# Optimization experiments

Hardware: AMD Instinct MI355X
Metric: run time of the kernel (lower is better)

Reference implementation:

```python
import jax, jax.numpy as jnp
import numpy as np

NO_FEATURES = 512
NO_HEADS = 8
HEAD_DIM = NO_FEATURES // NO_HEADS


def setup_inputs() -> dict:
    key = jax.random.key(0)
    ks = jax.random.split(key, 10)
    B, S, D = 4, 2048, NO_FEATURES
    s = 1.0 / np.sqrt(D)
    return {
        "x": jax.random.normal(ks[0], (B, S, D), dtype=jnp.float32),
        "ln_gamma": jnp.ones((D,), jnp.float32),
        "ln_beta": jnp.zeros((D,), jnp.float32),
        "Wq": jax.random.uniform(ks[1], (D, D), jnp.float32, -s, s),
        "bq": jax.random.uniform(ks[2], (D,), jnp.float32, -s, s),
        "Wk": jax.random.uniform(ks[3], (D, D), jnp.float32, -s, s),
        "bk": jax.random.uniform(ks[4], (D,), jnp.float32, -s, s),
        "Wv": jax.random.uniform(ks[5], (D, D), jnp.float32, -s, s),
        "bv": jax.random.uniform(ks[6], (D,), jnp.float32, -s, s),
        "Wo": jax.random.uniform(ks[7], (D, D), jnp.float32, -s, s),
        "bo": jax.random.uniform(ks[8], (D,), jnp.float32, -s, s),
    }


def reference(x, ln_gamma, ln_beta, Wq, bq, Wk, bk, Wv, bv, Wo, bo):
    B, S, D = x.shape
    H, Dh = NO_HEADS, D // NO_HEADS
    # Pre-LayerNorm (eps = 1e-5, torch default)
    mu = jnp.mean(x, axis=-1, keepdims=True)
    var = jnp.mean(jnp.square(x - mu), axis=-1, keepdims=True)
    xn = (x - mu) * jax.lax.rsqrt(var + 1e-5) * ln_gamma + ln_beta
    # QKV projections (torch Linear: x @ W.T + b)
    q = (xn @ Wq.T + bq).reshape(B, S, H, Dh).transpose(0, 2, 1, 3)
    k = (xn @ Wk.T + bk).reshape(B, S, H, Dh).transpose(0, 2, 1, 3)
    v = (xn @ Wv.T + bv).reshape(B, S, H, Dh).transpose(0, 2, 1, 3)
    scale = Dh ** -0.5
    scores = jnp.einsum("bhqd,bhkd->bhqk", q, k) * scale  # [B,H,S,S]
    attn = jax.nn.softmax(scores, axis=-1)
    # dropout is identity in eval mode
    out = jnp.einsum("bhqk,bhkd->bhqd", attn, v)
    out = out.transpose(0, 2, 1, 3).reshape(B, S, D)
    return out @ Wo.T + bo
```

## Files before the change

### kernel.cpp

```cpp
#include <hip/hip_runtime.h>
#include <cstdint>
#include <cstddef>

#define NB 4
#define NS 2048
#define ND 512
#define NH 8
#define DH 64
#define MTOK (NB*NS)

typedef __bf16 bf16x8 __attribute__((ext_vector_type(8)));
typedef float f32x4 __attribute__((ext_vector_type(4)));
typedef float f32x16 __attribute__((ext_vector_type(16)));
typedef unsigned int u32x4 __attribute__((ext_vector_type(4)));
typedef unsigned short ushort_t;
typedef unsigned int uint_t;

__device__ __forceinline__ unsigned short f2bf(float f) {
  unsigned int u = __builtin_bit_cast(unsigned int, f);
  return (unsigned short)((u + 0x7fffu + ((u >> 16) & 1u)) >> 16);
}

__device__ __forceinline__ uint_t cvtpk(float lo, float hi) {
  uint_t r;
  asm("v_cvt_pk_bf16_f32 %0, %1, %2" : "=v"(r) : "v"(lo), "v"(hi));
  return r;
}

__device__ __forceinline__ void pswap(uint_t &a, uint_t &b) {
  asm("v_permlane32_swap_b32 %0, %1" : "+v"(a), "+v"(b));
}

__device__ __forceinline__ void gload_lds16(const void* g, void* l) {
  __builtin_amdgcn_global_load_lds(
      (const __attribute__((address_space(1))) unsigned int*)g,
      (__attribute__((address_space(3))) unsigned int*)l,
      16, 0, 0);
}

__device__ __forceinline__ bf16x8 ld8(const ushort_t* p) { return *(const bf16x8*)p; }

__global__ __launch_bounds__(256) void ln_kernel(
    const float* __restrict__ x, const float* __restrict__ gamma,
    const float* __restrict__ beta, ushort_t* __restrict__ xn)
{
  const int row  = blockIdx.x * 4 + (threadIdx.x >> 6);
  const int lane = threadIdx.x & 63;
  const float4* xr = (const float4*)(x + (size_t)row * ND);
  float4 a = xr[lane*2], b = xr[lane*2+1];
  float v[8] = {a.x,a.y,a.z,a.w,b.x,b.y,b.z,b.w};
  float s = 0.f, s2 = 0.f;
#pragma unroll
  for (int j = 0; j < 8; ++j) { s += v[j]; s2 += v[j]*v[j]; }
#pragma unroll
  for (int mk = 1; mk < 64; mk <<= 1) { s += __shfl_xor(s, mk); s2 += __shfl_xor(s2, mk); }
  const float mu = s * (1.0f/ND);
  const float rs = rsqrtf(s2*(1.0f/ND) - mu*mu + 1e-5f);
  const float4* g4 = (const float4*)gamma;
  const float4* b4 = (const float4*)beta;
  float4 g0 = g4[lane*2], g1 = g4[lane*2+1];
  float4 e0 = b4[lane*2], e1 = b4[lane*2+1];
  float gv[8] = {g0.x,g0.y,g0.z,g0.w,g1.x,g1.y,g1.z,g1.w};
  float ev[8] = {e0.x,e0.y,e0.z,e0.w,e1.x,e1.y,e1.z,e1.w};
  unsigned short o[8];
#pragma unroll
  for (int j = 0; j < 8; ++j) o[j] = f2bf((v[j]-mu)*rs*gv[j] + ev[j]);
  uint4 ov;
  ov.x = (uint_t)o[0] | ((uint_t)o[1]<<16);
  ov.y = (uint_t)o[2] | ((uint_t)o[3]<<16);
  ov.z = (uint_t)o[4] | ((uint_t)o[5]<<16);
  ov.w = (uint_t)o[6] | ((uint_t)o[7]<<16);
  ((uint4*)(xn + (size_t)row*ND))[lane] = ov;
}

__global__ __launch_bounds__(256) void convert_w(
    const float* __restrict__ Wq, const float* __restrict__ Wk,
    const float* __restrict__ Wv, const float* __restrict__ Wo,
    ushort_t* __restrict__ wqkv, ushort_t* __restrict__ wob)
{
  const int t = blockIdx.x*256 + threadIdx.x;
  const int i = t*8;
  const float* src; ushort_t* dst;
  if (i < 1536*512) {
    const int n = i >> 9, c = i & 511;
    const float* W = (n < 512) ? Wq : (n < 1024) ? Wk : Wv;
    src = W + ((size_t)(n & 511) << 9) + c;
    dst = wqkv + i;
  } else {
    const int jj = i - 1536*512;
    src = Wo + jj; dst = wob + jj;
  }
  float4 a = ((const float4*)src)[0], b = ((const float4*)src)[1];
  uint4 o;
  o.x = (uint_t)f2bf(a.x) | ((uint_t)f2bf(a.y)<<16);
  o.y = (uint_t)f2bf(a.z) | ((uint_t)f2bf(a.w)<<16);
  o.z = (uint_t)f2bf(b.x) | ((uint_t)f2bf(b.y)<<16);
  o.w = (uint_t)f2bf(b.z) | ((uint_t)f2bf(b.w)<<16);
  *(uint4*)dst = o;
}

template<int EPI>
__global__ __launch_bounds__(256, 2) void gemm_bt(
    const ushort_t* __restrict__ A, const ushort_t* __restrict__ Bw, int Kd,
    const float* __restrict__ bq, const float* __restrict__ bk, const float* __restrict__ bv,
    ushort_t* __restrict__ qa, ushort_t* __restrict__ ka, ushort_t* __restrict__ vta,
    const float* __restrict__ bo, float* __restrict__ outp)
{
  __shared__ ushort_t lA[128*32];
  __shared__ ushort_t lB[128*32];
  const int tid = threadIdx.x;
  const int wave = tid >> 6, lane = tid & 63;
  const int m0 = blockIdx.y * 128, n0 = blockIdx.x * 128;
  const int wr = (wave >> 1) * 64, wc = (wave & 1) * 64;

  f32x4 acc[4][4] = {};

  const ushort_t* aS = A  + (size_t)(m0 + tid/4) * Kd + (tid & 3) * 8;
  const ushort_t* bS = Bw + (size_t)(n0 + tid/4) * Kd + (tid & 3) * 8;
  const size_t half = (size_t)64 * Kd;

  for (int k0 = 0; k0 < Kd; k0 += 32) {
    __syncthreads();
    gload_lds16(aS + k0,        lA + wave*512);
    gload_lds16(aS + half + k0, lA + 2048 + wave*512);
    gload_lds16(bS + k0,        lB + wave*512);
    gload_lds16(bS + half + k0, lB + 2048 + wave*512);
    __syncthreads();
    bf16x8 af[4], bfr[4];
#pragma unroll
    for (int i = 0; i < 4; ++i)
      af[i] = *(const bf16x8*)(lA + (wr + i*16 + (lane&15))*32 + (lane>>4)*8);
#pragma unroll
    for (int j = 0; j < 4; ++j)
      bfr[j] = *(const bf16x8*)(lB + (wc + j*16 + (lane&15))*32 + (lane>>4)*8);
#pragma unroll
    for (int i = 0; i < 4; ++i)
#pragma unroll
      for (int j = 0; j < 4; ++j)
        acc[i][j] = __builtin_amdgcn_mfma_f32_16x16x32_bf16(af[i], bfr[j], acc[i][j], 0, 0, 0);
  }

  if (EPI == 0) {
    const float QSCALE = 0.18033688011112042f;
#pragma unroll
    for (int j = 0; j < 4; ++j) {
      const int n = n0 + wc + j*16 + (lane & 15);
      const int which = n >> 9;
      const int nn = n & 511;
      const int h = nn >> 6, d = nn & 63;
      const float bb = (which == 0) ? bq[nn] : (which == 1) ? bk[nn] : bv[nn];
#pragma unroll
      for (int i = 0; i < 4; ++i)
#pragma unroll
        for (int r = 0; r < 4; ++r) {
          const int mm = m0 + wr + i*16 + 4*(lane>>4) + r;
          const int b = mm >> 11, s = mm & 2047;
          const int bh = b*NH + h;
          const float av = acc[i][j][r] + bb;
          if (which == 0) {
            qa[(((size_t)bh*64 + (s>>5))*4 + (d>>4))*512
               + (((d>>3)&1)*32 + (s&31))*8 + (d&7)] = f2bf(av * QSCALE);
          } else if (which == 1) {
            ka[(((size_t)bh*64 + (s>>5))*4 + (d>>4))*512
               + (((d>>3)&1)*32 + (s&31))*8 + (d&7)] = f2bf(av);
          } else {
            vta[(((size_t)bh*128 + (s>>4))*2 + (d>>5))*512
               + (((s>>3)&1)*32 + (d&31))*8 + (s&7)] = f2bf(av);
          }
        }
    }
  } else {
#pragma unroll
    for (int j = 0; j < 4; ++j) {
      const int n = n0 + wc + j*16 + (lane & 15);
      const float bb = bo[n];
#pragma unroll
      for (int i = 0; i < 4; ++i)
#pragma unroll
        for (int r = 0; r < 4; ++r) {
          const int m = m0 + wr + i*16 + 4*(lane>>4) + r;
          outp[(size_t)m*ND + n] = acc[i][j][r] + bb;
        }
    }
  }
}

__global__ __launch_bounds__(256) void attn_kernel(
    const ushort_t* __restrict__ qfv, const ushort_t* __restrict__ kfv,
    const ushort_t* __restrict__ vfv, ushort_t* __restrict__ ao)
{
  const int blk  = blockIdx.x;
  const int bh   = (blk & 7) | ((blk >> 7) << 3);
  const int qblk = (blk >> 3) & 15;
  const int w    = threadIdx.x >> 6;
  const int lane = threadIdx.x & 63;
  const int lo5 = lane & 31, hi = lane >> 5;
  const int qt = qblk*4 + w;

  const ushort_t* qb = qfv + (((size_t)bh*64 + qt)*4)*512 + lane*8;
  bf16x8 qf[4];
#pragma unroll
  for (int s = 0; s < 4; ++s) qf[s] = ld8(qb + s*512);

  const ushort_t* kb = kfv + ((size_t)bh*64*4)*512 + lane*8;
  const ushort_t* vb = vfv + ((size_t)bh*128*2)*512 + lane*8;

  f32x16 o0 = {}, o1 = {};
  float l0 = 0.f, l1 = 0.f, l2 = 0.f, l3 = 0.f;

  bf16x8 kf0[4], kf1[4];
#pragma unroll
  for (int s = 0; s < 4; ++s) {
    kf0[s] = ld8(kb + (size_t)s*512);
    kf1[s] = ld8(kb + (size_t)(4+s)*512);
  }

  for (int j0 = 0; j0 < NS; j0 += 64) {
    bf16x8 vf0[4], vf1[4];
    const int kv16 = j0 >> 4;
#pragma unroll
    for (int ks = 0; ks < 4; ++ks) {
      vf0[ks] = ld8(vb + ((size_t)(kv16+ks)*2    )*512);
      vf1[ks] = ld8(vb + ((size_t)(kv16+ks)*2 + 1)*512);
    }
    f32x16 s0 = {}, s1 = {};
#pragma unroll
    for (int s = 0; s < 4; ++s) {
      s0 = __builtin_amdgcn_mfma_f32_32x32x16_bf16(kf0[s], qf[s], s0, 0, 0, 0);
      s1 = __builtin_amdgcn_mfma_f32_32x32x16_bf16(kf1[s], qf[s], s1, 0, 0, 0);
    }
    if (j0 + 64 < NS) {
      const int kt = (j0 >> 5) + 2;
#pragma unroll
      for (int s = 0; s < 4; ++s) {
        kf0[s] = ld8(kb + ((size_t)(kt  )*4 + s)*512);
        kf1[s] = ld8(kb + ((size_t)(kt+1)*4 + s)*512);
      }
    }
#pragma unroll
    for (int r = 0; r < 16; r += 4) {
      s0[r]   = __builtin_amdgcn_exp2f(s0[r]);   l0 += s0[r];
      s0[r+1] = __builtin_amdgcn_exp2f(s0[r+1]); l1 += s0[r+1];
      s0[r+2] = __builtin_amdgcn_exp2f(s0[r+2]); l2 += s0[r+2];
      s0[r+3] = __builtin_amdgcn_exp2f(s0[r+3]); l3 += s0[r+3];
    }
#pragma unroll
    for (int r = 0; r < 16; r += 4) {
      s1[r]   = __builtin_amdgcn_exp2f(s1[r]);   l0 += s1[r];
      s1[r+1] = __builtin_amdgcn_exp2f(s1[r+1]); l1 += s1[r+1];
      s1[r+2] = __builtin_amdgcn_exp2f(s1[r+2]); l2 += s1[r+2];
      s1[r+3] = __builtin_amdgcn_exp2f(s1[r+3]); l3 += s1[r+3];
    }
    bf16x8 pf[4];
    {
      uint_t a, b, c, d;
      a = cvtpk(s0[0],  s0[1]);  b = cvtpk(s0[4],  s0[5]);  pswap(a, b);
      c = cvtpk(s0[2],  s0[3]);  d = cvtpk(s0[6],  s0[7]);  pswap(c, d);
      pf[0] = __builtin_bit_cast(bf16x8, (u32x4){a, c, b, d});
      a = cvtpk(s0[8],  s0[9]);  b = cvtpk(s0[12], s0[13]); pswap(a, b);
      c = cvtpk(s0[10], s0[11]); d = cvtpk(s0[14], s0[15]); pswap(c, d);
      pf[1] = __builtin_bit_cast(bf16x8, (u32x4){a, c, b, d});
      a = cvtpk(s1[0],  s1[1]);  b = cvtpk(s1[4],  s1[5]);  pswap(a, b);
      c = cvtpk(s1[2],  s1[3]);  d = cvtpk(s1[6],  s1[7]);  pswap(c, d);
      pf[2] = __builtin_bit_cast(bf16x8, (u32x4){a, c, b, d});
      a = cvtpk(s1[8],  s1[9]);  b = cvtpk(s1[12], s1[13]); pswap(a, b);
      c = cvtpk(s1[10], s1[11]); d = cvtpk(s1[14], s1[15]); pswap(c, d);
      pf[3] = __builtin_bit_cast(bf16x8, (u32x4){a, c, b, d});
    }
#pragma unroll
    for (int ks = 0; ks < 4; ++ks) {
      o0 = __builtin_amdgcn_mfma_f32_32x32x16_bf16(vf0[ks], pf[ks], o0, 0, 0, 0);
      o1 = __builtin_amdgcn_mfma_f32_32x32x16_bf16(vf1[ks], pf[ks], o1, 0, 0, 0);
    }
  }

  float l = (l0 + l1) + (l2 + l3);
  l += __shfl_xor(l, 32);
  const float rl = __builtin_amdgcn_rcpf(l);
  const int b = bh >> 3, h = bh & 7;
  const int srow = qt*32 + lo5;
  ushort_t* ob = ao + ((size_t)(b*NS + srow))*ND + h*DH;
#pragma unroll
  for (int dt = 0; dt < 2; ++dt) {
    f32x16& oo = dt ? o1 : o0;
#pragma unroll
    for (int r = 0; r < 16; r += 2) {
      const int d = (r & 3) + 8*(r >> 2) + 4*hi + dt*32;
      *(uint_t*)(ob + d) = cvtpk(oo[r]*rl, oo[r+1]*rl);
    }
  }
}

extern "C" void kernel_launch(void* const* d_in, const int* in_sizes, int n_in,
                              void* d_out, int out_size, void* d_ws, size_t ws_size,
                              hipStream_t stream)
{
  const float* x  = (const float*)d_in[0];
  const float* g  = (const float*)d_in[1];
  const float* be = (const float*)d_in[2];
  const float* Wq = (const float*)d_in[3];
  const float* bq = (const float*)d_in[4];
  const float* Wk = (const float*)d_in[5];
  const float* bk = (const float*)d_in[6];
  const float* Wv = (const float*)d_in[7];
  const float* bv = (const float*)d_in[8];
  const float* Wo = (const float*)d_in[9];
  const float* bo = (const float*)d_in[10];
  float* out = (float*)d_out;

  char* w = (char*)d_ws;
  ushort_t* xn   = (ushort_t*)w; w += (size_t)MTOK*ND*2;
  ushort_t* wqkv = (ushort_t*)w; w += (size_t)1536*512*2;
  ushort_t* wob  = (ushort_t*)w; w += (size_t)512*512*2;
  ushort_t* qa   = (ushort_t*)w; w += (size_t)MTOK*ND*2;
  ushort_t* ka   = (ushort_t*)w; w += (size_t)MTOK*ND*2;
  ushort_t* vta  = (ushort_t*)w; w += (size_t)MTOK*ND*2;
  ushort_t* ao   = (ushort_t*)w; w += (size_t)MTOK*ND*2;

  ln_kernel<<<MTOK/4, 256, 0, stream>>>(x, g, be, xn);
  convert_w<<<512, 256, 0, stream>>>(Wq, Wk, Wv, Wo, wqkv, wob);
  gemm_bt<0><<<dim3(12, 64), 256, 0, stream>>>(xn, wqkv, ND,
      bq, bk, bv, qa, ka, vta, nullptr, nullptr);
  attn_kernel<<<512, 256, 0, stream>>>(qa, ka, vta, ao);
  gemm_bt<1><<<dim3(4, 64), 256, 0, stream>>>(ao, wob, ND,
      nullptr, nullptr, nullptr, nullptr, nullptr, nullptr, bo, out);
}
```

Measured before the change: 100.9 us.

## Split attention over the key dimension into two halves with a combine pass

The attention kernel now splits each head's key range in two, launching twice as many blocks. Each block writes unnormalised fp32 partial outputs and row sums. A new combine kernel adds the partials, normalises them and writes bf16 output into the reused Q buffer; the final output buffer serves as scratch for one partial. This raises block count to fill more compute units, at the cost of extra fp32 traffic and one more launch. No running max is kept, which is fine because the pre-split code also skipped max subtraction.

```diff
diff --git a/kernel.cpp b/kernel.cpp
--- a/kernel.cpp
+++ b/kernel.cpp
@@ -8,6 +8,7 @@
 #define NH 8
 #define DH 64
 #define MTOK (NB*NS)
+#define NROW (NB*NH*NS)
 
 typedef __bf16 bf16x8 __attribute__((ext_vector_type(8)));
 typedef float f32x4 __attribute__((ext_vector_type(4)));
@@ -187,13 +188,15 @@
 
 __global__ __launch_bounds__(256) void attn_kernel(
     const ushort_t* __restrict__ qfv, const ushort_t* __restrict__ kfv,
-    const ushort_t* __restrict__ vfv, ushort_t* __restrict__ ao)
-{
-  const int blk  = blockIdx.x;
-  const int bh   = (blk & 7) | ((blk >> 7) << 3);
-  const int qblk = (blk >> 3) & 15;
-  const int w    = threadIdx.x >> 6;
-  const int lane = threadIdx.x & 63;
+    const ushort_t* __restrict__ vfv, float* __restrict__ op0,
+    float* __restrict__ op1, float* __restrict__ lsum)
+{
+  const int blk   = blockIdx.x;
+  const int bh    = (blk & 7) | ((blk >> 8) << 3);
+  const int qblk  = (blk >> 3) & 15;
+  const int split = (blk >> 7) & 1;
+  const int w     = threadIdx.x >> 6;
+  const int lane  = threadIdx.x & 63;
   const int lo5 = lane & 31, hi = lane >> 5;
   const int qt = qblk*4 + w;
 
@@ -202,8 +205,8 @@
 #pragma unroll
   for (int s = 0; s < 4; ++s) qf[s] = ld8(qb + s*512);
 
-  const ushort_t* kb = kfv + ((size_t)bh*64*4)*512 + lane*8;
-  const ushort_t* vb = vfv + ((size_t)bh*128*2)*512 + lane*8;
+  const ushort_t* kb = kfv + ((size_t)bh*256 + split*128)*512 + lane*8;
+  const ushort_t* vb = vfv + ((size_t)bh*256 + split*128)*512 + lane*8;
 
   f32x16 o0 = {}, o1 = {};
   float l0 = 0.f, l1 = 0.f, l2 = 0.f, l3 = 0.f;
@@ -215,7 +218,7 @@
     kf1[s] = ld8(kb + (size_t)(4+s)*512);
   }
 
-  for (int j0 = 0; j0 < NS; j0 += 64) {
+  for (int j0 = 0; j0 < NS/2; j0 += 64) {
     bf16x8 vf0[4], vf1[4];
     const int kv16 = j0 >> 4;
 #pragma unroll
@@ -229,7 +232,7 @@
       s0 = __builtin_amdgcn_mfma_f32_32x32x16_bf16(kf0[s], qf[s], s0, 0, 0, 0);
       s1 = __builtin_amdgcn_mfma_f32_32x32x16_bf16(kf1[s], qf[s], s1, 0, 0, 0);
     }
-    if (j0 + 64 < NS) {
+    if (j0 + 64 < NS/2) {
       const int kt = (j0 >> 5) + 2;
 #pragma unroll
       for (int s = 0; s < 4; ++s) {
@@ -276,19 +279,39 @@
 
   float l = (l0 + l1) + (l2 + l3);
   l += __shfl_xor(l, 32);
-  const float rl = __builtin_amdgcn_rcpf(l);
-  const int b = bh >> 3, h = bh & 7;
-  const int srow = qt*32 + lo5;
-  ushort_t* ob = ao + ((size_t)(b*NS + srow))*ND + h*DH;
+  const int row = bh*NS + qt*32 + lo5;
+  float* ob = (split ? op1 : op0) + (size_t)row * DH;
 #pragma unroll
   for (int dt = 0; dt < 2; ++dt) {
     f32x16& oo = dt ? o1 : o0;
 #pragma unroll
     for (int r = 0; r < 16; r += 2) {
       const int d = (r & 3) + 8*(r >> 2) + 4*hi + dt*32;
-      *(uint_t*)(ob + d) = cvtpk(oo[r]*rl, oo[r+1]*rl);
-    }
-  }
+      float2 v2; v2.x = oo[r]; v2.y = oo[r+1];
+      *(float2*)(ob + d) = v2;
+    }
+  }
+  if (hi == 0) lsum[(size_t)split*NROW + row] = l;
+}
+
+__global__ __launch_bounds__(256) void combine_kernel(
+    const float* __restrict__ op0, const float* __restrict__ op1,
+    const float* __restrict__ lsum, ushort_t* __restrict__ ao)
+{
+  const int t = blockIdx.x*256 + threadIdx.x;
+  const int row = t >> 3, d8 = (t & 7) * 8;
+  const float rl = 1.0f / (lsum[row] + lsum[NROW + row]);
+  const float4 a0 = *(const float4*)(op0 + (size_t)row*DH + d8);
+  const float4 a1 = *(const float4*)(op0 + (size_t)row*DH + d8 + 4);
+  const float4 b0 = *(const float4*)(op1 + (size_t)row*DH + d8);
+  const float4 b1 = *(const float4*)(op1 + (size_t)row*DH + d8 + 4);
+  u32x4 o;
+  o[0] = cvtpk((a0.x+b0.x)*rl, (a0.y+b0.y)*rl);
+  o[1] = cvtpk((a0.z+b0.z)*rl, (a0.w+b0.w)*rl);
+  o[2] = cvtpk((a1.x+b1.x)*rl, (a1.y+b1.y)*rl);
+  o[3] = cvtpk((a1.z+b1.z)*rl, (a1.w+b1.w)*rl);
+  const int bh = row >> 11, s = row & 2047, bb = bh >> 3, h = bh & 7;
+  *(u32x4*)(ao + ((size_t)(bb*NS + s))*ND + h*DH + d8) = o;
 }
 
 extern "C" void kernel_launch(void* const* d_in, const int* in_sizes, int n_in,
@@ -315,13 +338,17 @@
   ushort_t* qa   = (ushort_t*)w; w += (size_t)MTOK*ND*2;
   ushort_t* ka   = (ushort_t*)w; w += (size_t)MTOK*ND*2;
   ushort_t* vta  = (ushort_t*)w; w += (size_t)MTOK*ND*2;
-  ushort_t* ao   = (ushort_t*)w; w += (size_t)MTOK*ND*2;
+  float*    lsum = (float*)w;    w += (size_t)2*NROW*4;
+  float*    op1  = (float*)w;    w += (size_t)NROW*DH*4;
+  float* op0 = (float*)d_out;
+  ushort_t* ao = qa;
 
   ln_kernel<<<MTOK/4, 256, 0, stream>>>(x, g, be, xn);
   convert_w<<<512, 256, 0, stream>>>(Wq, Wk, Wv, Wo, wqkv, wob);
   gemm_bt<0><<<dim3(12, 64), 256, 0, stream>>>(xn, wqkv, ND,
       bq, bk, bv, qa, ka, vta, nullptr, nullptr);
-  attn_kernel<<<512, 256, 0, stream>>>(qa, ka, vta, ao);
+  attn_kernel<<<1024, 256, 0, stream>>>(qa, ka, vta, op0, op1, lsum);
+  combine_kernel<<<NROW*8/256, 256, 0, stream>>>(op0, op1, lsum, ao);
   gemm_bt<1><<<dim3(4, 64), 256, 0, stream>>>(ao, wob, ND,
       nullptr, nullptr, nullptr, nullptr, nullptr, nullptr, bo, out);
 }
```

Measured after the change: 109.5 us. 1.08x slower.

## Software-pipeline attention loop: overlap next QK MFMA with current softmax and PV

Applied to the files above, without the earlier changes.

Restructures the attention inner loop into a two-stage software pipeline with double-buffered score accumulators, so the QK^T MFMA for the next KV tile is issued before the exp/pack and PV MFMA of the current tile. K and V fragment loads are also moved to sit between pipeline stages. The aim is to hide MFMA latency behind the VALU softmax work and to keep loads in flight for longer. In exchange, register pressure rises from the extra score accumulators, which could cut occupancy or cause spills.

```diff
diff --git a/kernel.cpp b/kernel.cpp
--- a/kernel.cpp
+++ b/kernel.cpp
@@ -185,6 +185,70 @@
   }
 }
 
+__device__ __forceinline__ void load_k(bf16x8* kf0, bf16x8* kf1,
+                                       const ushort_t* kb, int t) {
+#pragma unroll
+  for (int s = 0; s < 4; ++s) {
+    kf0[s] = ld8(kb + ((size_t)(8*t + s))*512);
+    kf1[s] = ld8(kb + ((size_t)(8*t + 4 + s))*512);
+  }
+}
+__device__ __forceinline__ void load_v(bf16x8* vf0, bf16x8* vf1,
+                                       const ushort_t* vb, int t) {
+#pragma unroll
+  for (int ks = 0; ks < 4; ++ks) {
+    vf0[ks] = ld8(vb + ((size_t)(4*t + ks)*2    )*512);
+    vf1[ks] = ld8(vb + ((size_t)(4*t + ks)*2 + 1)*512);
+  }
+}
+__device__ __forceinline__ void qk_step(f32x16& s0, f32x16& s1,
+    const bf16x8* kf0, const bf16x8* kf1, const bf16x8* qf) {
+  s0 = {}; s1 = {};
+#pragma unroll
+  for (int s = 0; s < 4; ++s) {
+    s0 = __builtin_amdgcn_mfma_f32_32x32x16_bf16(kf0[s], qf[s], s0, 0, 0, 0);
+    s1 = __builtin_amdgcn_mfma_f32_32x32x16_bf16(kf1[s], qf[s], s1, 0, 0, 0);
+  }
+}
+__device__ __forceinline__ void softmax_pack(f32x16& s0, f32x16& s1, bf16x8* pf,
+    float& l0, float& l1, float& l2, float& l3) {
+#pragma unroll
+  for (int r = 0; r < 16; r += 4) {
+    s0[r]   = __builtin_amdgcn_exp2f(s0[r]);   l0 += s0[r];
+    s0[r+1] = __builtin_amdgcn_exp2f(s0[r+1]); l1 += s0[r+1];
+    s0[r+2] = __builtin_amdgcn_exp2f(s0[r+2]); l2 += s0[r+2];
+    s0[r+3] = __builtin_amdgcn_exp2f(s0[r+3]); l3 += s0[r+3];
+  }
+#pragma unroll
+  for (int r = 0; r < 16; r += 4) {
+    s1[r]   = __builtin_amdgcn_exp2f(s1[r]);   l0 += s1[r];
+    s1[r+1] = __builtin_amdgcn_exp2f(s1[r+1]); l1 += s1[r+1];
+    s1[r+2] = __builtin_amdgcn_exp2f(s1[r+2]); l2 += s1[r+2];
+    s1[r+3] = __builtin_amdgcn_exp2f(s1[r+3]); l3 += s1[r+3];
+  }
+  uint_t a, b, c, d;
+  a = cvtpk(s0[0],  s0[1]);  b = cvtpk(s0[4],  s0[5]);  pswap(a, b);
+  c = cvtpk(s0[2],  s0[3]);  d = cvtpk(s0[6],  s0[7]);  pswap(c, d);
+  pf[0] = __builtin_bit_cast(bf16x8, (u32x4){a, c, b, d});
+  a = cvtpk(s0[8],  s0[9]);  b = cvtpk(s0[12], s0[13]); pswap(a, b);
+  c = cvtpk(s0[10], s0[11]); d = cvtpk(s0[14], s0[15]); pswap(c, d);
+  pf[1] = __builtin_bit_cast(bf16x8, (u32x4){a, c, b, d});
+  a = cvtpk(s1[0],  s1[1]);  b = cvtpk(s1[4],  s1[5]);  pswap(a, b);
+  c = cvtpk(s1[2],  s1[3]);  d = cvtpk(s1[6],  s1[7]);  pswap(c, d);
+  pf[2] = __builtin_bit_cast(bf16x8, (u32x4){a, c, b, d});
+  a = cvtpk(s1[8],  s1[9]);  b = cvtpk(s1[12], s1[13]); pswap(a, b);
+  c = cvtpk(s1[10], s1[11]); d = cvtpk(s1[14], s1[15]); pswap(c, d);
+  pf[3] = __builtin_bit_cast(bf16x8, (u32x4){a, c, b, d});
+}
+__device__ __forceinline__ void pv_step(f32x16& o0, f32x16& o1,
+    const bf16x8* vf0, const bf16x8* vf1, const bf16x8* pf) {
+#pragma unroll
+  for (int ks = 0; ks < 4; ++ks) {
+    o0 = __builtin_amdgcn_mfma_f32_32x32x16_bf16(vf0[ks], pf[ks], o0, 0, 0, 0);
+    o1 = __builtin_amdgcn_mfma_f32_32x32x16_bf16(vf1[ks], pf[ks], o1, 0, 0, 0);
+  }
+}
+
 __global__ __launch_bounds__(256) void attn_kernel(
     const ushort_t* __restrict__ qfv, const ushort_t* __restrict__ kfv,
     const ushort_t* __restrict__ vfv, ushort_t* __restrict__ ao)
@@ -202,76 +266,49 @@
 #pragma unroll
   for (int s = 0; s < 4; ++s) qf[s] = ld8(qb + s*512);
 
-  const ushort_t* kb = kfv + ((size_t)bh*64*4)*512 + lane*8;
-  const ushort_t* vb = vfv + ((size_t)bh*128*2)*512 + lane*8;
+  const ushort_t* kb = kfv + ((size_t)bh*256)*512 + lane*8;
+  const ushort_t* vb = vfv + ((size_t)bh*256)*512 + lane*8;
 
   f32x16 o0 = {}, o1 = {};
+  f32x16 sA0 = {}, sA1 = {}, sB0 = {}, sB1 = {};
   float l0 = 0.f, l1 = 0.f, l2 = 0.f, l3 = 0.f;
-
-  bf16x8 kf0[4], kf1[4];
-#pragma unroll
-  for (int s = 0; s < 4; ++s) {
-    kf0[s] = ld8(kb + (size_t)s*512);
-    kf1[s] = ld8(kb + (size_t)(4+s)*512);
-  }
-
-  for (int j0 = 0; j0 < NS; j0 += 64) {
-    bf16x8 vf0[4], vf1[4];
-    const int kv16 = j0 >> 4;
-#pragma unroll
-    for (int ks = 0; ks < 4; ++ks) {
-      vf0[ks] = ld8(vb + ((size_t)(kv16+ks)*2    )*512);
-      vf1[ks] = ld8(vb + ((size_t)(kv16+ks)*2 + 1)*512);
-    }
-    f32x16 s0 = {}, s1 = {};
-#pragma unroll
-    for (int s = 0; s < 4; ++s) {
-      s0 = __builtin_amdgcn_mfma_f32_32x32x16_bf16(kf0[s], qf[s], s0, 0, 0, 0);
-      s1 = __builtin_amdgcn_mfma_f32_32x32x16_bf16(kf1[s], qf[s], s1, 0, 0, 0);
-    }
-    if (j0 + 64 < NS) {
-      const int kt = (j0 >> 5) + 2;
-#pragma unroll
-      for (int s = 0; s < 4; ++s) {
-        kf0[s] = ld8(kb + ((size_t)(kt  )*4 + s)*512);
-        kf1[s] = ld8(kb + ((size_t)(kt+1)*4 + s)*512);
-      }
-    }
-#pragma unroll
-    for (int r = 0; r < 16; r += 4) {
-      s0[r]   = __builtin_amdgcn_exp2f(s0[r]);   l0 += s0[r];
-      s0[r+1] = __builtin_amdgcn_exp2f(s0[r+1]); l1 += s0[r+1];
-      s0[r+2] = __builtin_amdgcn_exp2f(s0[r+2]); l2 += s0[r+2];
-      s0[r+3] = __builtin_amdgcn_exp2f(s0[r+3]); l3 += s0[r+3];
-    }
-#pragma unroll
-    for (int r = 0; r < 16; r += 4) {
-      s1[r]   = __builtin_amdgcn_exp2f(s1[r]);   l0 += s1[r];
-      s1[r+1] = __builtin_amdgcn_exp2f(s1[r+1]); l1 += s1[r+1];
-      s1[r+2] = __builtin_amdgcn_exp2f(s1[r+2]); l2 += s1[r+2];
-      s1[r+3] = __builtin_amdgcn_exp2f(s1[r+3]); l3 += s1[r+3];
-    }
+  bf16x8 kf0[4], kf1[4], vf0[4], vf1[4];
+
+  load_k(kf0, kf1, kb, 0);
+  load_v(vf0, vf1, vb, 0);
+  qk_step(sA0, sA1, kf0, kf1, qf);
+  load_k(kf0, kf1, kb, 1);
+
+  for (int i = 0; i < 15; ++i) {
+    const int t = 2*i;
+    qk_step(sB0, sB1, kf0, kf1, qf);
+    load_k(kf0, kf1, kb, t+2);
+    {
+      bf16x8 pf[4];
+      softmax_pack(sA0, sA1, pf, l0, l1, l2, l3);
+      pv_step(o0, o1, vf0, vf1, pf);
+    }
+    load_v(vf0, vf1, vb, t+1);
+    qk_step(sA0, sA1, kf0, kf1, qf);
+    load_k(kf0, kf1, kb, t+3);
+    {
+      bf16x8 pf[4];
+      softmax_pack(sB0, sB1, pf, l0, l1, l2, l3);
+      pv_step(o0, o1, vf0, vf1, pf);
+    }
+    load_v(vf0, vf1, vb, t+2);
+  }
+  qk_step(sB0, sB1, kf0, kf1, qf);
+  {
     bf16x8 pf[4];
-    {
-      uint_t a, b, c, d;
-      a = cvtpk(s0[0],  s0[1]);  b = cvtpk(s0[4],  s0[5]);  pswap(a, b);
-      c = cvtpk(s0[2],  s0[3]);  d = cvtpk(s0[6],  s0[7]);  pswap(c, d);
-      pf[0] = __builtin_bit_cast(bf16x8, (u32x4){a, c, b, d});
-      a = cvtpk(s0[8],  s0[9]);  b = cvtpk(s0[12], s0[13]); pswap(a, b);
-      c = cvtpk(s0[10], s0[11]); d = cvtpk(s0[14], s0[15]); pswap(c, d);
-      pf[1] = __builtin_bit_cast(bf16x8, (u32x4){a, c, b, d});
-      a = cvtpk(s1[0],  s1[1]);  b = cvtpk(s1[4],  s1[5]);  pswap(a, b);
-      c = cvtpk(s1[2],  s1[3]);  d = cvtpk(s1[6],  s1[7]);  pswap(c, d);
-      pf[2] = __builtin_bit_cast(bf16x8, (u32x4){a, c, b, d});
-      a = cvtpk(s1[8],  s1[9]);  b = cvtpk(s1[12], s1[13]); pswap(a, b);
-      c = cvtpk(s1[10], s1[11]); d = cvtpk(s1[14], s1[15]); pswap(c, d);
-      pf[3] = __builtin_bit_cast(bf16x8, (u32x4){a, c, b, d});
-    }
-#pragma unroll
-    for (int ks = 0; ks < 4; ++ks) {
-      o0 = __builtin_amdgcn_mfma_f32_32x32x16_bf16(vf0[ks], pf[ks], o0, 0, 0, 0);
-      o1 = __builtin_amdgcn_mfma_f32_32x32x16_bf16(vf1[ks], pf[ks], o1, 0, 0, 0);
-    }
+    softmax_pack(sA0, sA1, pf, l0, l1, l2, l3);
+    pv_step(o0, o1, vf0, vf1, pf);
+  }
+  load_v(vf0, vf1, vb, 31);
+  {
+    bf16x8 pf[4];
+    softmax_pack(sB0, sB1, pf, l0, l1, l2, l3);
+    pv_step(o0, o1, vf0, vf1, pf);
   }
 
   float l = (l0 + l1) + (l2 + l3);
```

Result: no change. 101.4 us (+0.5%).

## Double-buffer GEMM LDS tiles and add MFMA priority hints in attention

Applied to the files above, without the earlier changes.

The projection GEMM now keeps two LDS buffers and issues the next K-tile's global-to-LDS loads before computing on the current one. It waits with explicit vmcnt/lgkmcnt counts and raw barriers instead of two __syncthreads per iteration, so load latency can overlap the MFMA work. The attention kernel wraps its MFMA groups in s_setprio, seeds the first score MFMA from a zero constant, and accumulates the row sums as a vector add. The costs are double the GEMM LDS use, which may affect occupancy at 2 blocks per CU, and correctness that depends on hand-written waitcnt values.

```diff
diff --git a/kernel.cpp b/kernel.cpp
--- a/kernel.cpp
+++ b/kernel.cpp
@@ -106,8 +106,8 @@
     ushort_t* __restrict__ qa, ushort_t* __restrict__ ka, ushort_t* __restrict__ vta,
     const float* __restrict__ bo, float* __restrict__ outp)
 {
-  __shared__ ushort_t lA[128*32];
-  __shared__ ushort_t lB[128*32];
+  __shared__ ushort_t lA[2][128*32];
+  __shared__ ushort_t lB[2][128*32];
   const int tid = threadIdx.x;
   const int wave = tid >> 6, lane = tid & 63;
   const int m0 = blockIdx.y * 128, n0 = blockIdx.x * 128;
@@ -118,27 +118,43 @@
   const ushort_t* aS = A  + (size_t)(m0 + tid/4) * Kd + (tid & 3) * 8;
   const ushort_t* bS = Bw + (size_t)(n0 + tid/4) * Kd + (tid & 3) * 8;
   const size_t half = (size_t)64 * Kd;
-
-  for (int k0 = 0; k0 < Kd; k0 += 32) {
-    __syncthreads();
-    gload_lds16(aS + k0,        lA + wave*512);
-    gload_lds16(aS + half + k0, lA + 2048 + wave*512);
-    gload_lds16(bS + k0,        lB + wave*512);
-    gload_lds16(bS + half + k0, lB + 2048 + wave*512);
-    __syncthreads();
+  const int NT = Kd / 32;
+
+#define STAGE(BUF, K0)                                            \
+  gload_lds16(aS + (K0),        lA[BUF] + wave*512);              \
+  gload_lds16(aS + half + (K0), lA[BUF] + 2048 + wave*512);       \
+  gload_lds16(bS + (K0),        lB[BUF] + wave*512);              \
+  gload_lds16(bS + half + (K0), lB[BUF] + 2048 + wave*512);
+
+  STAGE(0, 0);
+  int cur = 0;
+  for (int t = 0; t < NT; ++t) {
+    if (t + 1 < NT) {
+      STAGE(cur ^ 1, (t + 1) * 32);
+      asm volatile("s_waitcnt vmcnt(4)" ::: "memory");
+    } else {
+      asm volatile("s_waitcnt vmcnt(0)" ::: "memory");
+    }
+    __builtin_amdgcn_s_barrier();
+    asm volatile("" ::: "memory");
     bf16x8 af[4], bfr[4];
 #pragma unroll
     for (int i = 0; i < 4; ++i)
-      af[i] = *(const bf16x8*)(lA + (wr + i*16 + (lane&15))*32 + (lane>>4)*8);
+      af[i] = *(const bf16x8*)(lA[cur] + (wr + i*16 + (lane&15))*32 + (lane>>4)*8);
 #pragma unroll
     for (int j = 0; j < 4; ++j)
-      bfr[j] = *(const bf16x8*)(lB + (wc + j*16 + (lane&15))*32 + (lane>>4)*8);
+      bfr[j] = *(const bf16x8*)(lB[cur] + (wc + j*16 + (lane&15))*32 + (lane>>4)*8);
 #pragma unroll
     for (int i = 0; i < 4; ++i)
 #pragma unroll
       for (int j = 0; j < 4; ++j)
         acc[i][j] = __builtin_amdgcn_mfma_f32_16x16x32_bf16(af[i], bfr[j], acc[i][j], 0, 0, 0);
-  }
+    asm volatile("s_waitcnt lgkmcnt(0)" ::: "memory");
+    __builtin_amdgcn_s_barrier();
+    asm volatile("" ::: "memory");
+    cur ^= 1;
+  }
+#undef STAGE
 
   if (EPI == 0) {
     const float QSCALE = 0.18033688011112042f;
@@ -202,11 +218,12 @@
 #pragma unroll
   for (int s = 0; s < 4; ++s) qf[s] = ld8(qb + s*512);
 
-  const ushort_t* kb = kfv + ((size_t)bh*64*4)*512 + lane*8;
-  const ushort_t* vb = vfv + ((size_t)bh*128*2)*512 + lane*8;
+  const ushort_t* kb = kfv + ((size_t)bh*256)*512 + lane*8;
+  const ushort_t* vb = vfv + ((size_t)bh*256)*512 + lane*8;
 
   f32x16 o0 = {}, o1 = {};
-  float l0 = 0.f, l1 = 0.f, l2 = 0.f, l3 = 0.f;
+  f32x16 lsv = {};
+  const f32x16 FZ = {};
 
   bf16x8 kf0[4], kf1[4];
 #pragma unroll
@@ -223,12 +240,16 @@
       vf0[ks] = ld8(vb + ((size_t)(kv16+ks)*2    )*512);
       vf1[ks] = ld8(vb + ((size_t)(kv16+ks)*2 + 1)*512);
     }
-    f32x16 s0 = {}, s1 = {};
-#pragma unroll
-    for (int s = 0; s < 4; ++s) {
+    f32x16 s0, s1;
+    __builtin_amdgcn_s_setprio(1);
+    s0 = __builtin_amdgcn_mfma_f32_32x32x16_bf16(kf0[0], qf[0], FZ, 0, 0, 0);
+    s1 = __builtin_amdgcn_mfma_f32_32x32x16_bf16(kf1[0], qf[0], FZ, 0, 0, 0);
+#pragma unroll
+    for (int s = 1; s < 4; ++s) {
       s0 = __builtin_amdgcn_mfma_f32_32x32x16_bf16(kf0[s], qf[s], s0, 0, 0, 0);
       s1 = __builtin_amdgcn_mfma_f32_32x32x16_bf16(kf1[s], qf[s], s1, 0, 0, 0);
     }
+    __builtin_amdgcn_s_setprio(0);
     if (j0 + 64 < NS) {
       const int kt = (j0 >> 5) + 2;
 #pragma unroll
@@ -238,19 +259,11 @@
       }
     }
 #pragma unroll
-    for (int r = 0; r < 16; r += 4) {
-      s0[r]   = __builtin_amdgcn_exp2f(s0[r]);   l0 += s0[r];
-      s0[r+1] = __builtin_amdgcn_exp2f(s0[r+1]); l1 += s0[r+1];
-      s0[r+2] = __builtin_amdgcn_exp2f(s0[r+2]); l2 += s0[r+2];
-      s0[r+3] = __builtin_amdgcn_exp2f(s0[r+3]); l3 += s0[r+3];
-    }
-#pragma unroll
-    for (int r = 0; r < 16; r += 4) {
-      s1[r]   = __builtin_amdgcn_exp2f(s1[r]);   l0 += s1[r];
-      s1[r+1] = __builtin_amdgcn_exp2f(s1[r+1]); l1 += s1[r+1];
-      s1[r+2] = __builtin_amdgcn_exp2f(s1[r+2]); l2 += s1[r+2];
-      s1[r+3] = __builtin_amdgcn_exp2f(s1[r+3]); l3 += s1[r+3];
-    }
+    for (int r = 0; r < 16; ++r) s0[r] = __builtin_amdgcn_exp2f(s0[r]);
+    lsv += s0;
+#pragma unroll
+    for (int r = 0; r < 16; ++r) s1[r] = __builtin_amdgcn_exp2f(s1[r]);
+    lsv += s1;
     bf16x8 pf[4];
     {
       uint_t a, b, c, d;
@@ -267,14 +280,18 @@
       c = cvtpk(s1[10], s1[11]); d = cvtpk(s1[14], s1[15]); pswap(c, d);
       pf[3] = __builtin_bit_cast(bf16x8, (u32x4){a, c, b, d});
     }
+    __builtin_amdgcn_s_setprio(1);
 #pragma unroll
     for (int ks = 0; ks < 4; ++ks) {
       o0 = __builtin_amdgcn_mfma_f32_32x32x16_bf16(vf0[ks], pf[ks], o0, 0, 0, 0);
       o1 = __builtin_amdgcn_mfma_f32_32x32x16_bf16(vf1[ks], pf[ks], o1, 0, 0, 0);
     }
-  }
-
-  float l = (l0 + l1) + (l2 + l3);
+    __builtin_amdgcn_s_setprio(0);
+  }
+
+  float l = 0.f;
+#pragma unroll
+  for (int r = 0; r < 16; ++r) l += lsv[r];
   l += __shfl_xor(l, 32);
   const float rl = __builtin_amdgcn_rcpf(l);
   const int b = bh >> 3, h = bh & 7;
```

Result: slower. 103.1 us (+2.1%).
